# Performance work log

Hardware: AMD Instinct MI355X
Metric: run time of the kernel (lower is better)

The kernel has to match this reference:

```python
import jax, jax.numpy as jnp
import numpy as np

N = 50000      # nodes
E = 1600000    # edges (avg degree 32)
F = 64         # input node features
H = 128        # GAT hidden dim (heads=1)
A = 16         # action dim
ED = 2         # edge feature dim


def setup_inputs() -> dict:
    key = jax.random.key(0)
    ks = jax.random.split(key, 20)
    def w(k, shape, fan_in):
        return jax.random.normal(k, shape, jnp.float32) * (1.0 / np.sqrt(fan_in))
    return {
        "x": jax.random.normal(ks[0], (N, F), jnp.float32),
        "edge_index": jax.random.randint(ks[1], (2, E), 0, N, dtype=jnp.int32),
        "edge_attr": jax.random.normal(ks[2], (E, ED), jnp.float32),
        # GATConv layer 1 (F -> H)
        "W1": w(ks[3], (F, H), F),
        "We1": w(ks[4], (ED, H), ED),
        "asrc1": w(ks[5], (H,), H),
        "adst1": w(ks[6], (H,), H),
        "aedge1": w(ks[7], (H,), H),
        "b1": jnp.zeros((H,), jnp.float32),
        # GATConv layer 2 (H -> H)
        "W2": w(ks[8], (H, H), H),
        "We2": w(ks[9], (ED, H), ED),
        "asrc2": w(ks[10], (H,), H),
        "adst2": w(ks[11], (H,), H),
        "aedge2": w(ks[12], (H,), H),
        "b2": jnp.zeros((H,), jnp.float32),
        # final head
        "Wfc": w(ks[13], (H, A), H),
        "bfc": jnp.zeros((A,), jnp.float32),
    }


def _gat_layer(x, src, dst, ea, W, We, a_s, a_d, a_e, b, n):
    """PyG GATConv, heads=1: gather -> attn logits -> segment softmax -> scatter-add."""
    h = x @ W                      # [n, H]
    he = ea @ We                   # [E', H]
    logits = jax.nn.leaky_relu(
        (h * a_s).sum(-1)[src] + (h * a_d).sum(-1)[dst] + (he * a_e).sum(-1),
        negative_slope=0.2,
    )                              # [E']
    m = jax.ops.segment_max(logits, dst, num_segments=n)
    p = jnp.exp(logits - m[dst])
    denom = jax.ops.segment_sum(p, dst, num_segments=n)
    alpha = p / (denom[dst] + 1e-16)
    out = jax.ops.segment_sum(h[src] * alpha[:, None], dst, num_segments=n)
    return out + b


def reference(x, edge_index, edge_attr, W1, We1, asrc1, adst1, aedge1, b1,
              W2, We2, asrc2, adst2, aedge2, b2, Wfc, bfc):
    n = x.shape[0]
    src0, dst0 = edge_index[0], edge_index[1]
    # add_self_loops=True with fill_value='mean': self-loop edge_attr is the
    # mean of incoming edge_attr per destination node (0 if no incoming edges)
    cnt = jax.ops.segment_sum(jnp.ones_like(dst0, dtype=edge_attr.dtype), dst0, num_segments=n)
    ea_mean = jax.ops.segment_sum(edge_attr, dst0, num_segments=n) / jnp.maximum(cnt, 1.0)[:, None]
    loops = jnp.arange(n, dtype=src0.dtype)
    src = jnp.concatenate([src0, loops])
    dst = jnp.concatenate([dst0, loops])
    ea = jnp.concatenate([edge_attr, ea_mean], axis=0)

    h = jax.nn.relu(_gat_layer(x, src, dst, ea, W1, We1, asrc1, adst1, aedge1, b1, n))
    h = jax.nn.relu(_gat_layer(h, src, dst, ea, W2, We2, asrc2, adst2, aedge2, b2, n))
    pooled = h.mean(axis=0)        # [H]
    return jnp.tanh(pooled @ Wfc + bfc)
```

## Files before the change

kernel.cpp:

```cpp
#include <hip/hip_runtime.h>
#include <hip/hip_fp16.h>
#include <math.h>

#define H_DIM 128
#define BWID 128
#define BMAX 512
#define CHUNK 4096

__global__ void prep_kernel(const float* __restrict__ We1, const float* __restrict__ ae1,
                            const float* __restrict__ We2, const float* __restrict__ ae2,
                            const float* __restrict__ W1, const float* __restrict__ as1,
                            const float* __restrict__ ad1,
                            const float* __restrict__ W2, const float* __restrict__ as2,
                            const float* __restrict__ ad2,
                            float* __restrict__ c, float* __restrict__ vs1,
                            float* __restrict__ vd1, float* __restrict__ vs2,
                            float* __restrict__ vd2) {
    int t = threadIdx.x;
    if (t < 64) {
        float s = 0.f, d = 0.f;
        for (int h = 0; h < 128; ++h) {
            float w = W1[t * 128 + h];
            s += w * as1[h];
            d += w * ad1[h];
        }
        vs1[t] = s; vd1[t] = d;
    } else if (t < 192) {
        int k = t - 64;
        float s = 0.f, d = 0.f;
        for (int h = 0; h < 128; ++h) {
            float w = W2[k * 128 + h];
            s += w * as2[h];
            d += w * ad2[h];
        }
        vs2[k] = s; vd2[k] = d;
    } else {
        int l = t - 192;
        float a1x = ae1[l], a1y = ae1[l + 64];
        float a2x = ae2[l], a2y = ae2[l + 64];
        float v0 = We1[l] * a1x + We1[l + 64] * a1y;
        float v1 = We1[128 + l] * a1x + We1[192 + l] * a1y;
        float v2 = We2[l] * a2x + We2[l + 64] * a2y;
        float v3 = We2[128 + l] * a2x + We2[192 + l] * a2y;
        for (int off = 32; off; off >>= 1) {
            v0 += __shfl_xor(v0, off);
            v1 += __shfl_xor(v1, off);
            v2 += __shfl_xor(v2, off);
            v3 += __shfl_xor(v3, off);
        }
        if (l == 0) { c[0] = v0; c[1] = v1; c[2] = v2; c[3] = v3; }
    }
}

__global__ __launch_bounds__(256) void count_kernel(const int* __restrict__ ei,
                                                    int* __restrict__ gcnt, int E, int B) {
    __shared__ int hist[BMAX];
    int tid = threadIdx.x;
    for (int i = tid; i < B; i += 256) hist[i] = 0;
    __syncthreads();
    int lo = blockIdx.x * CHUNK, hi = min(lo + CHUNK, E);
    for (int e = lo + tid; e < hi; e += 256)
        atomicAdd(&hist[ei[E + e] >> 7], 1);
    __syncthreads();
    for (int i = tid; i < B; i += 256)
        if (hist[i]) atomicAdd(&gcnt[i], hist[i]);
}

__global__ void bscan_kernel(const int* __restrict__ gcnt, int* __restrict__ bstart,
                             int* __restrict__ gcur, int* __restrict__ rowptr,
                             int B, int n, int E) {
    __shared__ int s[BMAX];
    int t = threadIdx.x;
    int v0 = (t < B) ? gcnt[t] : 0;
    s[t] = v0;
    __syncthreads();
    for (int off = 1; off < BMAX; off <<= 1) {
        int v = (t >= off) ? s[t - off] : 0;
        __syncthreads();
        s[t] += v;
        __syncthreads();
    }
    if (t < B) {
        int excl = s[t] - v0;
        bstart[t] = excl;
        gcur[t] = excl;
    }
    if (t == 0) { bstart[B] = E; rowptr[n] = E; }
}

__global__ __launch_bounds__(256) void bin_kernel(const int* __restrict__ ei,
                                                  const float* __restrict__ ea,
                                                  const float* __restrict__ cvec,
                                                  int* __restrict__ gcur,
                                                  int2* __restrict__ binned, int E, int B) {
    __shared__ int cnt[BMAX];
    __shared__ int base[BMAX];
    int tid = threadIdx.x;
    for (int i = tid; i < B; i += 256) cnt[i] = 0;
    __syncthreads();
    int lo = blockIdx.x * CHUNK, hi = min(lo + CHUNK, E);
    for (int e = lo + tid; e < hi; e += 256)
        atomicAdd(&cnt[ei[E + e] >> 7], 1);
    __syncthreads();
    for (int i = tid; i < B; i += 256) {
        int c = cnt[i];
        base[i] = c ? atomicAdd(&gcur[i], c) : 0;
        cnt[i] = 0;
    }
    __syncthreads();
    float c0 = cvec[0], c1 = cvec[1], c2 = cvec[2], c3 = cvec[3];
    for (int e = lo + tid; e < hi; e += 256) {
        int s = ei[e], d = ei[E + e];
        float2 v = ((const float2*)ea)[e];
        float d1 = c0 * v.x + c1 * v.y;
        float d2 = c2 * v.x + c3 * v.y;
        __half2 hh = __floats2half2_rn(d1, d2);
        int b = d >> 7;
        int loc = atomicAdd(&cnt[b], 1);
        binned[(size_t)(base[b] + loc)] = make_int2(s | ((d & 127) << 16), *(int*)&hh);
    }
}

__global__ __launch_bounds__(256) void build_kernel(const int* __restrict__ bstart,
                                                    const int2* __restrict__ binned,
                                                    int* __restrict__ rowptr,
                                                    int2* __restrict__ csr, int n) {
    __shared__ int cnt[BWID];
    __shared__ int sc[BWID];
    __shared__ int cur[BWID];
    int b = blockIdx.x, tid = threadIdx.x;
    int d0 = b << 7;
    int lo = bstart[b], hi = bstart[b + 1];
    if (tid < BWID) cnt[tid] = 0;
    __syncthreads();
    for (int k = lo + tid; k < hi; k += 256)
        atomicAdd(&cnt[(binned[k].x >> 16) & (BWID - 1)], 1);
    __syncthreads();
    if (tid < BWID) sc[tid] = cnt[tid];
    __syncthreads();
    for (int off = 1; off < BWID; off <<= 1) {
        int v = (tid < BWID && tid >= off) ? sc[tid - off] : 0;
        __syncthreads();
        if (tid < BWID) sc[tid] += v;
        __syncthreads();
    }
    if (tid < BWID) {
        int excl = sc[tid] - cnt[tid];
        cur[tid] = lo + excl;
        int d = d0 + tid;
        if (d < n) rowptr[d] = lo + excl;
    }
    __syncthreads();
    for (int k = lo + tid; k < hi; k += 256) {
        int2 e = binned[k];
        int slot = atomicAdd(&cur[(e.x >> 16) & (BWID - 1)], 1);
        csr[slot] = make_int2(e.x & 0xFFFF, e.y);
    }
}

__global__ void hshd64_kernel(const float* __restrict__ x, const float* __restrict__ vs,
                              const float* __restrict__ vd, float* __restrict__ hs,
                              float* __restrict__ hd, __half* __restrict__ xh, int n) {
    int w = (blockIdx.x * blockDim.x + threadIdx.x) >> 6;
    int lane = threadIdx.x & 63;
    if (w >= n) return;
    float xv = x[(size_t)w * 64 + lane];
    xh[(size_t)w * 64 + lane] = __float2half(xv);
    float ss = xv * vs[lane];
    float sd = xv * vd[lane];
    for (int off = 32; off; off >>= 1) {
        ss += __shfl_xor(ss, off);
        sd += __shfl_xor(sd, off);
    }
    if (lane == 0) { hs[w] = ss; hd[w] = sd; }
}

__global__ __launch_bounds__(256) void agg64_kernel(
        const int* __restrict__ rowptr, const int2* __restrict__ csr,
        const float* __restrict__ hs, const float* __restrict__ hd,
        const __half* __restrict__ feat, __half* __restrict__ t_out, int n) {
    int w = (blockIdx.x * blockDim.x + threadIdx.x) >> 6;
    int lane = threadIdx.x & 63;
    if (w >= n) return;
    int beg = rowptr[w], end = rowptr[w + 1];
    int len = end - beg;
    float hdv = hd[w], hsw = hs[w];
    int g = lane >> 4;
    int c16 = lane & 15;
    float4 acc = make_float4(0.f, 0.f, 0.f, 0.f);
    float m, scale, lself;

    if (len <= 64) {
        bool valid = lane < len;
        int2 c2 = valid ? csr[beg + lane] : make_int2(0, 0);
        __half2 dd = *(__half2*)&c2.y;
        float ed = valid ? __half2float(dd.x) : 0.f;
        float l = hs[c2.x] + hdv + ed;
        l = (l >= 0.f) ? l : 0.2f * l;
        float mymax = valid ? l : -1e30f;
        float edsum = ed;
        for (int off = 32; off; off >>= 1) {
            mymax = fmaxf(mymax, __shfl_xor(mymax, off));
            edsum += __shfl_xor(edsum, off);
        }
        lself = hsw + hdv + edsum / fmaxf((float)len, 1.0f);
        lself = (lself >= 0.f) ? lself : 0.2f * lself;
        m = fmaxf(mymax, lself);
        float p = valid ? __expf(l - m) : 0.f;
        float psum = p;
        for (int off = 32; off; off >>= 1) psum += __shfl_xor(psum, off);
        psum += __expf(lself - m);
        scale = 1.f / (psum + 1e-16f);
        float pn = p * scale;
        int src = c2.x;
        for (int j = g; j < len; j += 4) {
            float a = __shfl(pn, j);
            int sj = __shfl(src, j);
            float2 raw = *(const float2*)&feat[(size_t)sj * 64 + c16 * 4];
            __half2 h01 = *(__half2*)&raw.x;
            __half2 h23 = *(__half2*)&raw.y;
            float2 f01 = __half22float2(h01);
            float2 f23 = __half22float2(h23);
            acc.x += a * f01.x; acc.y += a * f01.y;
            acc.z += a * f23.x; acc.w += a * f23.y;
        }
    } else {
        float mymax = -1e30f, edsum = 0.f;
        for (int base = beg; base < end; base += 64) {
            int k = base + lane;
            if (k < end) {
                int2 c2 = csr[k];
                __half2 dd = *(__half2*)&c2.y;
                float ed = __half2float(dd.x);
                edsum += ed;
                float l = hs[c2.x] + hdv + ed;
                l = (l >= 0.f) ? l : 0.2f * l;
                mymax = fmaxf(mymax, l);
            }
        }
        for (int off = 32; off; off >>= 1) {
            mymax = fmaxf(mymax, __shfl_xor(mymax, off));
            edsum += __shfl_xor(edsum, off);
        }
        lself = hsw + hdv + edsum / fmaxf((float)len, 1.0f);
        lself = (lself >= 0.f) ? lself : 0.2f * lself;
        m = fmaxf(mymax, lself);
        float psum = 0.f;
        for (int base = beg; base < end; base += 64) {
            int k = base + lane;
            if (k < end) {
                int2 c2 = csr[k];
                __half2 dd = *(__half2*)&c2.y;
                float l = hs[c2.x] + hdv + __half2float(dd.x);
                l = (l >= 0.f) ? l : 0.2f * l;
                psum += __expf(l - m);
            }
        }
        for (int off = 32; off; off >>= 1) psum += __shfl_xor(psum, off);
        psum += __expf(lself - m);
        scale = 1.f / (psum + 1e-16f);
        for (int base = beg; base < end; base += 64) {
            int k = base + lane;
            float pn = 0.f; int src = 0;
            if (k < end) {
                int2 c2 = csr[k];
                __half2 dd = *(__half2*)&c2.y;
                float l = hs[c2.x] + hdv + __half2float(dd.x);
                l = (l >= 0.f) ? l : 0.2f * l;
                pn = __expf(l - m) * scale;
                src = c2.x;
            }
            int cl = min(end - base, 64);
            for (int j = g; j < cl; j += 4) {
                float a = __shfl(pn, j);
                int sj = __shfl(src, j);
                float2 raw = *(const float2*)&feat[(size_t)sj * 64 + c16 * 4];
                __half2 h01 = *(__half2*)&raw.x;
                __half2 h23 = *(__half2*)&raw.y;
                float2 f01 = __half22float2(h01);
                float2 f23 = __half22float2(h23);
                acc.x += a * f01.x; acc.y += a * f01.y;
                acc.z += a * f23.x; acc.w += a * f23.y;
            }
        }
    }
    if (g == 0) {
        float a = __expf(lself - m) * scale;
        float2 raw = *(const float2*)&feat[(size_t)w * 64 + c16 * 4];
        __half2 h01 = *(__half2*)&raw.x;
        __half2 h23 = *(__half2*)&raw.y;
        float2 f01 = __half22float2(h01);
        float2 f23 = __half22float2(h23);
        acc.x += a * f01.x; acc.y += a * f01.y;
        acc.z += a * f23.x; acc.w += a * f23.y;
    }
    float4 p1, p2, p3;
    p1.x = __shfl(acc.x, c16 + 16); p1.y = __shfl(acc.y, c16 + 16);
    p1.z = __shfl(acc.z, c16 + 16); p1.w = __shfl(acc.w, c16 + 16);
    p2.x = __shfl(acc.x, c16 + 32); p2.y = __shfl(acc.y, c16 + 32);
    p2.z = __shfl(acc.z, c16 + 32); p2.w = __shfl(acc.w, c16 + 32);
    p3.x = __shfl(acc.x, c16 + 48); p3.y = __shfl(acc.y, c16 + 48);
    p3.z = __shfl(acc.z, c16 + 48); p3.w = __shfl(acc.w, c16 + 48);
    if (lane < 16) {
        float4 o;
        o.x = acc.x + p1.x + p2.x + p3.x;
        o.y = acc.y + p1.y + p2.y + p3.y;
        o.z = acc.z + p1.z + p2.z + p3.z;
        o.w = acc.w + p1.w + p2.w + p3.w;
        __half2 q0 = __floats2half2_rn(o.x, o.y);
        __half2 q1 = __floats2half2_rn(o.z, o.w);
        int2 st; st.x = *(int*)&q0; st.y = *(int*)&q1;
        *(int2*)&t_out[(size_t)w * 64 + c16 * 4] = st;
    }
}

__global__ __launch_bounds__(256) void agg128_kernel(
        const int* __restrict__ rowptr, const int2* __restrict__ csr,
        const float* __restrict__ hs, const float* __restrict__ hd,
        const __half* __restrict__ feat, __half* __restrict__ t_out, int n) {
    int w = (blockIdx.x * blockDim.x + threadIdx.x) >> 6;
    int lane = threadIdx.x & 63;
    if (w >= n) return;
    int beg = rowptr[w], end = rowptr[w + 1];
    int len = end - beg;
    float hdv = hd[w], hsw = hs[w];
    int half = lane >> 5;
    int col = lane & 31;
    float4 acc = make_float4(0.f, 0.f, 0.f, 0.f);
    float m, scale, lself;

    if (len <= 64) {
        bool valid = lane < len;
        int2 c2 = valid ? csr[beg + lane] : make_int2(0, 0);
        __half2 dd = *(__half2*)&c2.y;
        float ed = valid ? __half2float(dd.y) : 0.f;
        float l = hs[c2.x] + hdv + ed;
        l = (l >= 0.f) ? l : 0.2f * l;
        float mymax = valid ? l : -1e30f;
        float edsum = ed;
        for (int off = 32; off; off >>= 1) {
            mymax = fmaxf(mymax, __shfl_xor(mymax, off));
            edsum += __shfl_xor(edsum, off);
        }
        lself = hsw + hdv + edsum / fmaxf((float)len, 1.0f);
        lself = (lself >= 0.f) ? lself : 0.2f * lself;
        m = fmaxf(mymax, lself);
        float p = valid ? __expf(l - m) : 0.f;
        float psum = p;
        for (int off = 32; off; off >>= 1) psum += __shfl_xor(psum, off);
        psum += __expf(lself - m);
        scale = 1.f / (psum + 1e-16f);
        float pn = p * scale;
        int src = c2.x;
        for (int j = half; j < len; j += 2) {
            float a = __shfl(pn, j);
            int sj = __shfl(src, j);
            float2 raw = *(const float2*)&feat[(size_t)sj * H_DIM + col * 4];
            __half2 h01 = *(__half2*)&raw.x;
            __half2 h23 = *(__half2*)&raw.y;
            float2 f01 = __half22float2(h01);
            float2 f23 = __half22float2(h23);
            acc.x += a * f01.x; acc.y += a * f01.y;
            acc.z += a * f23.x; acc.w += a * f23.y;
        }
    } else {
        float mymax = -1e30f, edsum = 0.f;
        for (int base = beg; base < end; base += 64) {
            int k = base + lane;
            if (k < end) {
                int2 c2 = csr[k];
                __half2 dd = *(__half2*)&c2.y;
                float ed = __half2float(dd.y);
                edsum += ed;
                float l = hs[c2.x] + hdv + ed;
                l = (l >= 0.f) ? l : 0.2f * l;
                mymax = fmaxf(mymax, l);
            }
        }
        for (int off = 32; off; off >>= 1) {
            mymax = fmaxf(mymax, __shfl_xor(mymax, off));
            edsum += __shfl_xor(edsum, off);
        }
        lself = hsw + hdv + edsum / fmaxf((float)len, 1.0f);
        lself = (lself >= 0.f) ? lself : 0.2f * lself;
        m = fmaxf(mymax, lself);
        float psum = 0.f;
        for (int base = beg; base < end; base += 64) {
            int k = base + lane;
            if (k < end) {
                int2 c2 = csr[k];
                __half2 dd = *(__half2*)&c2.y;
                float l = hs[c2.x] + hdv + __half2float(dd.y);
                l = (l >= 0.f) ? l : 0.2f * l;
                psum += __expf(l - m);
            }
        }
        for (int off = 32; off; off >>= 1) psum += __shfl_xor(psum, off);
        psum += __expf(lself - m);
        scale = 1.f / (psum + 1e-16f);
        for (int base = beg; base < end; base += 64) {
            int k = base + lane;
            float pn = 0.f; int src = 0;
            if (k < end) {
                int2 c2 = csr[k];
                __half2 dd = *(__half2*)&c2.y;
                float l = hs[c2.x] + hdv + __half2float(dd.y);
                l = (l >= 0.f) ? l : 0.2f * l;
                pn = __expf(l - m) * scale;
                src = c2.x;
            }
            int cl = min(end - base, 64);
            for (int j = half; j < cl; j += 2) {
                float a = __shfl(pn, j);
                int sj = __shfl(src, j);
                float2 raw = *(const float2*)&feat[(size_t)sj * H_DIM + col * 4];
                __half2 h01 = *(__half2*)&raw.x;
                __half2 h23 = *(__half2*)&raw.y;
                float2 f01 = __half22float2(h01);
                float2 f23 = __half22float2(h23);
                acc.x += a * f01.x; acc.y += a * f01.y;
                acc.z += a * f23.x; acc.w += a * f23.y;
            }
        }
    }
    if (half == 0) {
        float a = __expf(lself - m) * scale;
        float2 raw = *(const float2*)&feat[(size_t)w * H_DIM + col * 4];
        __half2 h01 = *(__half2*)&raw.x;
        __half2 h23 = *(__half2*)&raw.y;
        float2 f01 = __half22float2(h01);
        float2 f23 = __half22float2(h23);
        acc.x += a * f01.x; acc.y += a * f01.y;
        acc.z += a * f23.x; acc.w += a * f23.y;
    }
    float4 oth;
    oth.x = __shfl(acc.x, col + 32);
    oth.y = __shfl(acc.y, col + 32);
    oth.z = __shfl(acc.z, col + 32);
    oth.w = __shfl(acc.w, col + 32);
    if (half == 0) {
        float4 o;
        o.x = acc.x + oth.x; o.y = acc.y + oth.y;
        o.z = acc.z + oth.z; o.w = acc.w + oth.w;
        __half2 q0 = __floats2half2_rn(o.x, o.y);
        __half2 q1 = __floats2half2_rn(o.z, o.w);
        int2 st; st.x = *(int*)&q0; st.y = *(int*)&q1;
        *(int2*)&t_out[(size_t)w * H_DIM + col * 4] = st;
    }
}

template <int FIN, bool DO_HSHD, bool OUT_HALF, bool DO_POOL>
__global__ __launch_bounds__(256) void gemm_kernel(const __half* __restrict__ X,
                                                   const float* __restrict__ W,
                                                   const float* __restrict__ bias,
                                                   const float* __restrict__ vs,
                                                   const float* __restrict__ vd,
                                                   void* __restrict__ HoutV,
                                                   float* __restrict__ hs,
                                                   float* __restrict__ hd,
                                                   float* __restrict__ pooled, int n) {
    __shared__ float xs[32 * FIN];
    __shared__ float psum[DO_POOL ? 128 : 1];
    int tid = threadIdx.x;
    int r0 = blockIdx.x * 32;
    if (DO_POOL && tid < 128) psum[tid] = 0.f;
    constexpr int NV = 32 * FIN / 8;
    for (int idx = tid; idx < NV; idx += 256) {
        int r = (idx * 8) / FIN, k = idx * 8 - r * FIN;
        int row = r0 + r;
        float* p = &xs[r * FIN + k];
        if (row < n) {
            int4 raw = *(const int4*)&X[(size_t)row * FIN + k];
            __half2 h0 = *(__half2*)&raw.x;
            __half2 h1 = *(__half2*)&raw.y;
            __half2 h2 = *(__half2*)&raw.z;
            __half2 h3 = *(__half2*)&raw.w;
            float2 f0 = __half22float2(h0), f1 = __half22float2(h1);
            float2 f2 = __half22float2(h2), f3 = __half22float2(h3);
            p[0] = f0.x; p[1] = f0.y; p[2] = f1.x; p[3] = f1.y;
            p[4] = f2.x; p[5] = f2.y; p[6] = f3.x; p[7] = f3.y;
        } else {
#pragma unroll
            for (int q = 0; q < 8; ++q) p[q] = 0.f;
        }
    }
    __syncthreads();
    int tcol = tid & 31;
    int trow = tid >> 5;
    float acc[4][4] = {{0.f}};
    const float* wp = W + tcol * 4;
    const float* x0p = &xs[(trow * 4 + 0) * FIN];
    const float* x1p = &xs[(trow * 4 + 1) * FIN];
    const float* x2p = &xs[(trow * 4 + 2) * FIN];
    const float* x3p = &xs[(trow * 4 + 3) * FIN];
#pragma unroll 8
    for (int k = 0; k < FIN; ++k) {
        float4 w4 = *(const float4*)(wp + k * H_DIM);
        float x0 = x0p[k], x1 = x1p[k], x2 = x2p[k], x3 = x3p[k];
        acc[0][0] += x0 * w4.x; acc[0][1] += x0 * w4.y; acc[0][2] += x0 * w4.z; acc[0][3] += x0 * w4.w;
        acc[1][0] += x1 * w4.x; acc[1][1] += x1 * w4.y; acc[1][2] += x1 * w4.z; acc[1][3] += x1 * w4.w;
        acc[2][0] += x2 * w4.x; acc[2][1] += x2 * w4.y; acc[2][2] += x2 * w4.z; acc[2][3] += x2 * w4.w;
        acc[3][0] += x3 * w4.x; acc[3][1] += x3 * w4.y; acc[3][2] += x3 * w4.z; acc[3][3] += x3 * w4.w;
    }
    float4 b4 = *(const float4*)&bias[tcol * 4];
    float4 vs4, vd4;
    if (DO_HSHD) {
        vs4 = *(const float4*)&vs[tcol * 4];
        vd4 = *(const float4*)&vd[tcol * 4];
    }
    float cps0 = 0.f, cps1 = 0.f, cps2 = 0.f, cps3 = 0.f;
#pragma unroll
    for (int r = 0; r < 4; ++r) {
        int row = r0 + trow * 4 + r;
        float4 o;
        o.x = fmaxf(acc[r][0] + b4.x, 0.f);
        o.y = fmaxf(acc[r][1] + b4.y, 0.f);
        o.z = fmaxf(acc[r][2] + b4.z, 0.f);
        o.w = fmaxf(acc[r][3] + b4.w, 0.f);
        if (row < n) {
            if (DO_POOL) {
                cps0 += o.x; cps1 += o.y; cps2 += o.z; cps3 += o.w;
            } else if (OUT_HALF) {
                __half2 q0 = __floats2half2_rn(o.x, o.y);
                __half2 q1 = __floats2half2_rn(o.z, o.w);
                int2 st; st.x = *(int*)&q0; st.y = *(int*)&q1;
                *(int2*)((__half*)HoutV + (size_t)row * H_DIM + tcol * 4) = st;
            } else {
                *(float4*)((float*)HoutV + (size_t)row * H_DIM + tcol * 4) = o;
            }
        }
        if (DO_HSHD) {
            float ss = o.x * vs4.x + o.y * vs4.y + o.z * vs4.z + o.w * vs4.w;
            float sd = o.x * vd4.x + o.y * vd4.y + o.z * vd4.z + o.w * vd4.w;
            for (int off = 16; off; off >>= 1) {
                ss += __shfl_xor(ss, off);
                sd += __shfl_xor(sd, off);
            }
            if (tcol == 0 && row < n) { hs[row] = ss; hd[row] = sd; }
        }
    }
    if (DO_POOL) {
        atomicAdd(&psum[tcol * 4 + 0], cps0);
        atomicAdd(&psum[tcol * 4 + 1], cps1);
        atomicAdd(&psum[tcol * 4 + 2], cps2);
        atomicAdd(&psum[tcol * 4 + 3], cps3);
        __syncthreads();
        if (tid < 128) atomicAdd(&pooled[tid], psum[tid]);
    }
}

__global__ void final_kernel(const float* __restrict__ pooled, const float* __restrict__ Wfc,
                             const float* __restrict__ bfc, float* __restrict__ out, int n) {
    int t = threadIdx.x;
    if (t >= 16) return;
    float inv_n = 1.0f / (float)n;
    float s = 0.f;
    for (int j = 0; j < 128; ++j) s += pooled[j] * inv_n * Wfc[j * 16 + t];
    out[t] = tanhf(s + bfc[t]);
}

extern "C" void kernel_launch(void* const* d_in, const int* in_sizes, int n_in,
                              void* d_out, int out_size, void* d_ws, size_t ws_size,
                              hipStream_t stream) {
    const float* x   = (const float*)d_in[0];
    const int*   ei  = (const int*)d_in[1];
    const float* ea  = (const float*)d_in[2];
    const float* W1  = (const float*)d_in[3];
    const float* We1 = (const float*)d_in[4];
    const float* as1 = (const float*)d_in[5];
    const float* ad1 = (const float*)d_in[6];
    const float* ae1 = (const float*)d_in[7];
    const float* b1  = (const float*)d_in[8];
    const float* W2  = (const float*)d_in[9];
    const float* We2 = (const float*)d_in[10];
    const float* as2 = (const float*)d_in[11];
    const float* ad2 = (const float*)d_in[12];
    const float* ae2 = (const float*)d_in[13];
    const float* b2  = (const float*)d_in[14];
    const float* Wfc = (const float*)d_in[15];
    const float* bfc = (const float*)d_in[16];
    float* out = (float*)d_out;

    const int n = in_sizes[0] / 64;
    const int E = in_sizes[1] / 2;
    const int B = (n + BWID - 1) / BWID;

    size_t o = 0;
    auto alloc = [&](size_t count) { size_t r = o; o += (count + 63) & ~(size_t)63; return r; };
    size_t o_gcnt   = alloc(BMAX);
    size_t o_bstart = alloc(BMAX + 1);
    size_t o_gcur   = alloc(BMAX);
    size_t o_rowptr = alloc(n + 1);
    size_t o_csr    = alloc(2 * (size_t)E);
    size_t o_bufA   = alloc((size_t)n * H_DIM);
    size_t o_xh     = alloc((size_t)n * 32);
    size_t o_t1h    = alloc((size_t)n * 32);
    size_t o_o1h    = alloc((size_t)n * 64);
    size_t o_t2h    = alloc((size_t)n * 64);
    size_t o_hs     = alloc(n);
    size_t o_hd     = alloc(n);
    size_t o_c      = alloc(4);
    size_t o_vs1    = alloc(64);
    size_t o_vd1    = alloc(64);
    size_t o_vs2    = alloc(128);
    size_t o_vd2    = alloc(128);
    size_t o_pool   = alloc(128);
    (void)ws_size;
    float* wsf = (float*)d_ws;
    int2* binned = (int2*)(wsf + o_bufA);
    int2* csr2   = (int2*)(wsf + o_csr);

    hipMemsetAsync(wsf + o_gcnt, 0, BMAX * sizeof(int), stream);
    hipMemsetAsync(wsf + o_pool, 0, 128 * sizeof(float), stream);

    prep_kernel<<<1, 256, 0, stream>>>(We1, ae1, We2, ae2, W1, as1, ad1, W2, as2, ad2,
        wsf + o_c, wsf + o_vs1, wsf + o_vd1, wsf + o_vs2, wsf + o_vd2);

    int ebg = (E + CHUNK - 1) / CHUNK;
    count_kernel<<<ebg, 256, 0, stream>>>(ei, (int*)(wsf + o_gcnt), E, B);
    bscan_kernel<<<1, BMAX, 0, stream>>>((int*)(wsf + o_gcnt), (int*)(wsf + o_bstart),
        (int*)(wsf + o_gcur), (int*)(wsf + o_rowptr), B, n, E);
    bin_kernel<<<ebg, 256, 0, stream>>>(ei, ea, wsf + o_c, (int*)(wsf + o_gcur),
        binned, E, B);
    build_kernel<<<B, 256, 0, stream>>>((int*)(wsf + o_bstart), binned,
        (int*)(wsf + o_rowptr), csr2, n);

    int wgrid = (n + 3) / 4;

    hshd64_kernel<<<wgrid, 256, 0, stream>>>(x, wsf + o_vs1, wsf + o_vd1,
        wsf + o_hs, wsf + o_hd, (__half*)(wsf + o_xh), n);
    agg64_kernel<<<wgrid, 256, 0, stream>>>((int*)(wsf + o_rowptr), csr2,
        wsf + o_hs, wsf + o_hd, (const __half*)(wsf + o_xh), (__half*)(wsf + o_t1h), n);
    gemm_kernel<64, true, true, false><<<(n + 31) / 32, 256, 0, stream>>>(
        (const __half*)(wsf + o_t1h), W1, b1, wsf + o_vs2, wsf + o_vd2,
        (void*)(wsf + o_o1h), wsf + o_hs, wsf + o_hd, nullptr, n);

    agg128_kernel<<<wgrid, 256, 0, stream>>>((int*)(wsf + o_rowptr), csr2,
        wsf + o_hs, wsf + o_hd, (const __half*)(wsf + o_o1h), (__half*)(wsf + o_t2h), n);
    gemm_kernel<128, false, true, true><<<(n + 31) / 32, 256, 0, stream>>>(
        (const __half*)(wsf + o_t2h), W2, b2, nullptr, nullptr,
        nullptr, nullptr, nullptr, wsf + o_pool, n);

    final_kernel<<<1, 64, 0, stream>>>(wsf + o_pool, Wfc, bfc, out, n);
}
```

Measured before the change: 370.2 us.

## Replace two-level binned CSR build with direct global-atomic counting sort

Swaps the bucketed CSR construction (LDS histograms per 128-node bin, then a per-bin local sort) for a plain counting sort: per-destination global atomic counts, a three-kernel prefix scan over nodes, and a scatter that takes each slot with a global atomic on the destination cursor. This removes the intermediate binned buffer and one full pass over the edges. In exchange, every edge issues scattered global atomics instead of LDS atomics, and edge order within a row is no longer grouped by the source block. scan2 handles at most 64 blocks, which limits n to 65536.

```diff
diff --git a/kernel.cpp b/kernel.cpp
--- a/kernel.cpp
+++ b/kernel.cpp
@@ -3,9 +3,7 @@
 #include <math.h>
 
 #define H_DIM 128
-#define BWID 128
-#define BMAX 512
-#define CHUNK 4096
+#define SCAN_BLK 1024
 
 __global__ void prep_kernel(const float* __restrict__ We1, const float* __restrict__ ae1,
                             const float* __restrict__ We2, const float* __restrict__ ae2,
@@ -52,109 +50,95 @@
     }
 }
 
-__global__ __launch_bounds__(256) void count_kernel(const int* __restrict__ ei,
-                                                    int* __restrict__ gcnt, int E, int B) {
-    __shared__ int hist[BMAX];
-    int tid = threadIdx.x;
-    for (int i = tid; i < B; i += 256) hist[i] = 0;
+__global__ __launch_bounds__(256) void dcount_kernel(const int* __restrict__ ei,
+                                                     int* __restrict__ cnt, int E) {
+    int e = blockIdx.x * blockDim.x + threadIdx.x;
+    int st = gridDim.x * blockDim.x;
+    for (; e < E; e += st) atomicAdd(&cnt[ei[E + e]], 1);
+}
+
+__global__ __launch_bounds__(256) void scan1_kernel(const int* __restrict__ cnt,
+                                                    int* __restrict__ rowptr,
+                                                    int* __restrict__ bsum, int n) {
+    __shared__ int s[256];
+    int t = threadIdx.x;
+    int base = blockIdx.x * SCAN_BLK + t * 4;
+    int c0 = 0, c1 = 0, c2 = 0, c3 = 0;
+    if (base + 3 < n) {
+        int4 v = *(const int4*)&cnt[base];
+        c0 = v.x; c1 = v.y; c2 = v.z; c3 = v.w;
+    } else {
+        if (base + 0 < n) c0 = cnt[base + 0];
+        if (base + 1 < n) c1 = cnt[base + 1];
+        if (base + 2 < n) c2 = cnt[base + 2];
+        if (base + 3 < n) c3 = cnt[base + 3];
+    }
+    int tot = c0 + c1 + c2 + c3;
+    s[t] = tot;
     __syncthreads();
-    int lo = blockIdx.x * CHUNK, hi = min(lo + CHUNK, E);
-    for (int e = lo + tid; e < hi; e += 256)
-        atomicAdd(&hist[ei[E + e] >> 7], 1);
-    __syncthreads();
-    for (int i = tid; i < B; i += 256)
-        if (hist[i]) atomicAdd(&gcnt[i], hist[i]);
-}
-
-__global__ void bscan_kernel(const int* __restrict__ gcnt, int* __restrict__ bstart,
-                             int* __restrict__ gcur, int* __restrict__ rowptr,
-                             int B, int n, int E) {
-    __shared__ int s[BMAX];
-    int t = threadIdx.x;
-    int v0 = (t < B) ? gcnt[t] : 0;
-    s[t] = v0;
-    __syncthreads();
-    for (int off = 1; off < BMAX; off <<= 1) {
+    for (int off = 1; off < 256; off <<= 1) {
         int v = (t >= off) ? s[t - off] : 0;
         __syncthreads();
         s[t] += v;
         __syncthreads();
     }
-    if (t < B) {
-        int excl = s[t] - v0;
-        bstart[t] = excl;
-        gcur[t] = excl;
-    }
-    if (t == 0) { bstart[B] = E; rowptr[n] = E; }
-}
-
-__global__ __launch_bounds__(256) void bin_kernel(const int* __restrict__ ei,
-                                                  const float* __restrict__ ea,
-                                                  const float* __restrict__ cvec,
-                                                  int* __restrict__ gcur,
-                                                  int2* __restrict__ binned, int E, int B) {
-    __shared__ int cnt[BMAX];
-    __shared__ int base[BMAX];
-    int tid = threadIdx.x;
-    for (int i = tid; i < B; i += 256) cnt[i] = 0;
+    int excl = s[t] - tot;
+    if (base + 0 < n) rowptr[base + 0] = excl;
+    if (base + 1 < n) rowptr[base + 1] = excl + c0;
+    if (base + 2 < n) rowptr[base + 2] = excl + c0 + c1;
+    if (base + 3 < n) rowptr[base + 3] = excl + c0 + c1 + c2;
+    if (t == 255) bsum[blockIdx.x] = s[255];
+}
+
+__global__ void scan2_kernel(int* __restrict__ bsum, int nb) {
+    __shared__ int s[64];
+    int t = threadIdx.x;
+    int v = (t < nb) ? bsum[t] : 0;
+    s[t] = v;
     __syncthreads();
-    int lo = blockIdx.x * CHUNK, hi = min(lo + CHUNK, E);
-    for (int e = lo + tid; e < hi; e += 256)
-        atomicAdd(&cnt[ei[E + e] >> 7], 1);
-    __syncthreads();
-    for (int i = tid; i < B; i += 256) {
-        int c = cnt[i];
-        base[i] = c ? atomicAdd(&gcur[i], c) : 0;
-        cnt[i] = 0;
-    }
-    __syncthreads();
+    for (int off = 1; off < 64; off <<= 1) {
+        int u = (t >= off) ? s[t - off] : 0;
+        __syncthreads();
+        s[t] += u;
+        __syncthreads();
+    }
+    if (t < nb) bsum[t] = s[t] - v;
+}
+
+__global__ __launch_bounds__(256) void scan3_kernel(int* __restrict__ rowptr,
+                                                    int* __restrict__ cur,
+                                                    const int* __restrict__ bsum,
+                                                    int n, int E) {
+    int b = blockIdx.x;
+    int off = bsum[b];
+    int base = b * SCAN_BLK;
+    for (int i = threadIdx.x; i < SCAN_BLK; i += 256) {
+        int idx = base + i;
+        if (idx < n) {
+            int v = rowptr[idx] + off;
+            rowptr[idx] = v;
+            cur[idx] = v;
+        }
+    }
+    if (b == 0 && threadIdx.x == 0) rowptr[n] = E;
+}
+
+__global__ __launch_bounds__(256) void scatter_kernel(const int* __restrict__ ei,
+                                                      const float* __restrict__ ea,
+                                                      const float* __restrict__ cvec,
+                                                      int* __restrict__ cur,
+                                                      int2* __restrict__ csr, int E) {
     float c0 = cvec[0], c1 = cvec[1], c2 = cvec[2], c3 = cvec[3];
-    for (int e = lo + tid; e < hi; e += 256) {
+    int e = blockIdx.x * blockDim.x + threadIdx.x;
+    int st = gridDim.x * blockDim.x;
+    for (; e < E; e += st) {
         int s = ei[e], d = ei[E + e];
         float2 v = ((const float2*)ea)[e];
         float d1 = c0 * v.x + c1 * v.y;
         float d2 = c2 * v.x + c3 * v.y;
         __half2 hh = __floats2half2_rn(d1, d2);
-        int b = d >> 7;
-        int loc = atomicAdd(&cnt[b], 1);
-        binned[(size_t)(base[b] + loc)] = make_int2(s | ((d & 127) << 16), *(int*)&hh);
-    }
-}
-
-__global__ __launch_bounds__(256) void build_kernel(const int* __restrict__ bstart,
-                                                    const int2* __restrict__ binned,
-                                                    int* __restrict__ rowptr,
-                                                    int2* __restrict__ csr, int n) {
-    __shared__ int cnt[BWID];
-    __shared__ int sc[BWID];
-    __shared__ int cur[BWID];
-    int b = blockIdx.x, tid = threadIdx.x;
-    int d0 = b << 7;
-    int lo = bstart[b], hi = bstart[b + 1];
-    if (tid < BWID) cnt[tid] = 0;
-    __syncthreads();
-    for (int k = lo + tid; k < hi; k += 256)
-        atomicAdd(&cnt[(binned[k].x >> 16) & (BWID - 1)], 1);
-    __syncthreads();
-    if (tid < BWID) sc[tid] = cnt[tid];
-    __syncthreads();
-    for (int off = 1; off < BWID; off <<= 1) {
-        int v = (tid < BWID && tid >= off) ? sc[tid - off] : 0;
-        __syncthreads();
-        if (tid < BWID) sc[tid] += v;
-        __syncthreads();
-    }
-    if (tid < BWID) {
-        int excl = sc[tid] - cnt[tid];
-        cur[tid] = lo + excl;
-        int d = d0 + tid;
-        if (d < n) rowptr[d] = lo + excl;
-    }
-    __syncthreads();
-    for (int k = lo + tid; k < hi; k += 256) {
-        int2 e = binned[k];
-        int slot = atomicAdd(&cur[(e.x >> 16) & (BWID - 1)], 1);
-        csr[slot] = make_int2(e.x & 0xFFFF, e.y);
+        int slot = atomicAdd(&cur[d], 1);
+        csr[slot] = make_int2(s, *(int*)&hh);
     }
 }
 
@@ -583,16 +567,15 @@
 
     const int n = in_sizes[0] / 64;
     const int E = in_sizes[1] / 2;
-    const int B = (n + BWID - 1) / BWID;
+    const int NB = (n + SCAN_BLK - 1) / SCAN_BLK;
 
     size_t o = 0;
     auto alloc = [&](size_t count) { size_t r = o; o += (count + 63) & ~(size_t)63; return r; };
-    size_t o_gcnt   = alloc(BMAX);
-    size_t o_bstart = alloc(BMAX + 1);
-    size_t o_gcur   = alloc(BMAX);
+    size_t o_cnt    = alloc(n);
+    size_t o_cur    = alloc(n);
+    size_t o_bsum   = alloc(64);
     size_t o_rowptr = alloc(n + 1);
     size_t o_csr    = alloc(2 * (size_t)E);
-    size_t o_bufA   = alloc((size_t)n * H_DIM);
     size_t o_xh     = alloc((size_t)n * 32);
     size_t o_t1h    = alloc((size_t)n * 32);
     size_t o_o1h    = alloc((size_t)n * 64);
@@ -607,23 +590,22 @@
     size_t o_pool   = alloc(128);
     (void)ws_size;
     float* wsf = (float*)d_ws;
-    int2* binned = (int2*)(wsf + o_bufA);
-    int2* csr2   = (int2*)(wsf + o_csr);
-
-    hipMemsetAsync(wsf + o_gcnt, 0, BMAX * sizeof(int), stream);
+    int2* csr2 = (int2*)(wsf + o_csr);
+
+    hipMemsetAsync(wsf + o_cnt, 0, n * sizeof(int), stream);
     hipMemsetAsync(wsf + o_pool, 0, 128 * sizeof(float), stream);
 
     prep_kernel<<<1, 256, 0, stream>>>(We1, ae1, We2, ae2, W1, as1, ad1, W2, as2, ad2,
         wsf + o_c, wsf + o_vs1, wsf + o_vd1, wsf + o_vs2, wsf + o_vd2);
 
-    int ebg = (E + CHUNK - 1) / CHUNK;
-    count_kernel<<<ebg, 256, 0, stream>>>(ei, (int*)(wsf + o_gcnt), E, B);
-    bscan_kernel<<<1, BMAX, 0, stream>>>((int*)(wsf + o_gcnt), (int*)(wsf + o_bstart),
-        (int*)(wsf + o_gcur), (int*)(wsf + o_rowptr), B, n, E);
-    bin_kernel<<<ebg, 256, 0, stream>>>(ei, ea, wsf + o_c, (int*)(wsf + o_gcur),
-        binned, E, B);
-    build_kernel<<<B, 256, 0, stream>>>((int*)(wsf + o_bstart), binned,
-        (int*)(wsf + o_rowptr), csr2, n);
+    dcount_kernel<<<2048, 256, 0, stream>>>(ei, (int*)(wsf + o_cnt), E);
+    scan1_kernel<<<NB, 256, 0, stream>>>((int*)(wsf + o_cnt), (int*)(wsf + o_rowptr),
+        (int*)(wsf + o_bsum), n);
+    scan2_kernel<<<1, 64, 0, stream>>>((int*)(wsf + o_bsum), NB);
+    scan3_kernel<<<NB, 256, 0, stream>>>((int*)(wsf + o_rowptr), (int*)(wsf + o_cur),
+        (int*)(wsf + o_bsum), n, E);
+    scatter_kernel<<<2048, 256, 0, stream>>>(ei, ea, wsf + o_c, (int*)(wsf + o_cur),
+        csr2, E);
 
     int wgrid = (n + 3) / 4;
 
```

Result: slower. 504.8 us (+36.3%).
